# Performance work log

Hardware: AMD Instinct MI355X
Metric: run time of the kernel (lower is better)

## Reference

```python
import jax, jax.numpy as jnp
import numpy as np

B, T, H, W, C = 2, 8, 64, 64, 192
WIN = (4, 8, 8)
SHIFT = (2, 4, 4)
HEADS = 6
HID = 4 * C
N = WIN[0] * WIN[1] * WIN[2]  # 256 tokens per window
CPB_HID = 512


def window_partition(x, win):
    b, t, h, w, c = x.shape
    x = x.reshape(b, t // win[0], win[0], h // win[1], win[1], w // win[2], win[2], c)
    x = x.transpose(0, 1, 3, 5, 2, 4, 6, 7)
    return x.reshape(-1, win[0] * win[1] * win[2], c)


def window_reverse(wins, win, b, t, h, w):
    x = wins.reshape(b, t // win[0], h // win[1], w // win[2], win[0], win[1], win[2], -1)
    x = x.transpose(0, 1, 4, 2, 5, 3, 6, 7)
    return x.reshape(b, t, h, w, -1)


def _rel_coords_table():
    axes = [np.arange(-(WIN[i] - 1), WIN[i], dtype=np.float32) for i in range(3)]
    tbl = np.stack(np.meshgrid(*axes, indexing='ij'), axis=-1)  # (2wt-1,2wh-1,2ww-1,3)
    for i in range(3):
        tbl[..., i] /= WIN[i] - 1
    tbl *= 8.0
    tbl = np.sign(tbl) * np.log2(np.abs(tbl) + 1.0) / np.log2(8.0)
    return tbl.reshape(-1, 3)


def _rel_pos_index():
    coords = np.stack(np.meshgrid(np.arange(WIN[0]), np.arange(WIN[1]), np.arange(WIN[2]), indexing='ij'))
    cf = coords.reshape(3, -1)
    rel = (cf[:, :, None] - cf[:, None, :]).transpose(1, 2, 0)
    rel[..., 0] += WIN[0] - 1
    rel[..., 1] += WIN[1] - 1
    rel[..., 2] += WIN[2] - 1
    rel[..., 0] *= (2 * WIN[1] - 1) * (2 * WIN[2] - 1)
    rel[..., 1] *= 2 * WIN[2] - 1
    return rel.sum(-1)  # (N, N) int


def _attn_mask():
    img = np.zeros((1, T, H, W, 1), dtype=np.float32)
    cnt = 0
    for d in (slice(-WIN[0]), slice(-WIN[0], -SHIFT[0]), slice(-SHIFT[0], None)):
        for h in (slice(-WIN[1]), slice(-WIN[1], -SHIFT[1]), slice(-SHIFT[1], None)):
            for w in (slice(-WIN[2]), slice(-WIN[2], -SHIFT[2]), slice(-SHIFT[2], None)):
                img[:, d, h, w, :] = cnt
                cnt += 1
    mw = window_partition(img, WIN).squeeze(-1)  # (nW, N)
    am = mw[:, None, :] - mw[:, :, None]
    return np.where(am != 0, -100.0, 0.0).astype(np.float32)


REL_TABLE = jnp.asarray(_rel_coords_table())      # (M, 3)
RPI = jnp.asarray(_rel_pos_index().reshape(-1))   # (N*N,)
MASK = jnp.asarray(_attn_mask())                  # (nW, N, N)


def _ln(x, g, b):
    m = x.mean(-1, keepdims=True)
    v = x.var(-1, keepdims=True)
    return (x - m) / jnp.sqrt(v + 1e-5) * g + b


def setup_inputs() -> dict:
    key = jax.random.key(0)
    ks = jax.random.split(key, 16)
    s = lambda fan: 1.0 / np.sqrt(fan)
    return {
        'x': jax.random.normal(ks[0], (B, T, H, W, C), jnp.float32),
        'qkv_w': jax.random.normal(ks[1], (3 * C, C), jnp.float32) * s(C),
        'qkv_b': jnp.zeros((3 * C,), jnp.float32),
        'proj_w': jax.random.normal(ks[2], (C, C), jnp.float32) * s(C),
        'proj_b': jnp.zeros((C,), jnp.float32),
        'cpb_w1': jax.random.normal(ks[3], (CPB_HID, 3), jnp.float32) * s(3),
        'cpb_b1': jnp.zeros((CPB_HID,), jnp.float32),
        'cpb_w2': jax.random.normal(ks[4], (HEADS, CPB_HID), jnp.float32) * s(CPB_HID),
        'logit_scale': jnp.log(10.0 * jnp.ones((HEADS, 1, 1), jnp.float32)),
        'norm1_g': jnp.ones((C,), jnp.float32),
        'norm1_b': jnp.zeros((C,), jnp.float32),
        'norm2_g': jnp.ones((C,), jnp.float32),
        'norm2_b': jnp.zeros((C,), jnp.float32),
        'fc1_w': jax.random.normal(ks[5], (HID, C), jnp.float32) * s(C),
        'fc1_b': jnp.zeros((HID,), jnp.float32),
        'fc2_w': jax.random.normal(ks[6], (C, HID), jnp.float32) * s(HID),
        'fc2_b': jnp.zeros((C,), jnp.float32),
    }


def reference(x, qkv_w, qkv_b, proj_w, proj_b, cpb_w1, cpb_b1, cpb_w2,
              logit_scale, norm1_g, norm1_b, norm2_g, norm2_b,
              fc1_w, fc1_b, fc2_w, fc2_b):
    shortcut = x
    # cyclic shift
    xs = jnp.roll(x, shift=(-SHIFT[0], -SHIFT[1], -SHIFT[2]), axis=(1, 2, 3))
    xw = window_partition(xs, WIN)  # (B*nW, N, C)
    B_ = xw.shape[0]
    d = C // HEADS
    qkv = (xw @ qkv_w.T + qkv_b).reshape(B_, N, 3, HEADS, d).transpose(2, 0, 3, 1, 4)
    q, k, v = qkv[0], qkv[1], qkv[2]  # (B_, h, N, d)
    # cosine attention (F.normalize eps=1e-12)
    qn = q / jnp.maximum(jnp.linalg.norm(q, axis=-1, keepdims=True), 1e-12)
    kn = k / jnp.maximum(jnp.linalg.norm(k, axis=-1, keepdims=True), 1e-12)
    attn = jnp.einsum('bhnd,bhmd->bhnm', qn, kn)
    scale = jnp.exp(jnp.minimum(logit_scale, jnp.log(100.0)))  # clamp at log(1/0.01)
    attn = attn * scale
    # continuous relative position bias
    tbl = jax.nn.relu(REL_TABLE @ cpb_w1.T + cpb_b1) @ cpb_w2.T  # (M, heads)
    bias = tbl[RPI].reshape(N, N, HEADS).transpose(2, 0, 1)      # (h, N, N)
    attn = attn + 16.0 * jax.nn.sigmoid(bias)[None]
    # shift mask
    nW = MASK.shape[0]
    attn = attn.reshape(B_ // nW, nW, HEADS, N, N) + MASK[None, :, None]
    attn = jax.nn.softmax(attn.reshape(B_, HEADS, N, N), axis=-1)
    out = jnp.einsum('bhnm,bhmd->bhnd', attn, v)
    out = out.transpose(0, 2, 1, 3).reshape(B_, N, C)
    out = out @ proj_w.T + proj_b
    xr = window_reverse(out, WIN, B, T, H, W)
    xr = jnp.roll(xr, shift=SHIFT, axis=(1, 2, 3))
    # SwinV2 res-post-norm residual
    x = shortcut + _ln(xr, norm1_g, norm1_b)
    h1 = jax.nn.gelu(x @ fc1_w.T + fc1_b, approximate=False)
    x = x + _ln(h1 @ fc2_w.T + fc2_b, norm2_g, norm2_b)
    return x
```

## Files before the change

### kernel.cpp

```cpp
#include <hip/hip_runtime.h>
#include <math.h>


typedef short short8 __attribute__((ext_vector_type(8)));
typedef short short4v __attribute__((ext_vector_type(4)));
typedef float f32x4 __attribute__((ext_vector_type(4)));

__device__ __forceinline__ short f2bf(float f) {
    union { float f; unsigned u; } v; v.f = f;
    unsigned r = v.u + 0x7FFF + ((v.u >> 16) & 1);
    return (short)(r >> 16);
}

__device__ __forceinline__ float gelu_fast(float x) {
    float s = x * x;
    float t = fmaf(0.044715f, s, 1.0f);
    float y = -1.5957691216057308f * x * t;
    return x / (1.0f + __expf(y));
}

__global__ __launch_bounds__(64) void pack_w_k(const float* __restrict__ w,
                                               short* __restrict__ dst, int K) {
    int lane = threadIdx.x;
    int ktn = K >> 5;
    int nt = blockIdx.x / ktn, kt = blockIdx.x % ktn;
    int r = lane & 15, q = lane >> 4;
    const float* src = w + (size_t)(nt * 16 + r) * K + kt * 32 + q * 8;
    short8 v;
#pragma unroll
    for (int j = 0; j < 8; j++) v[j] = f2bf(src[j]);
    ((short8*)dst)[(size_t)blockIdx.x * 64 + lane] = v;
}

__global__ __launch_bounds__(64) void cpb_table_k(const float* __restrict__ w1,
                                                  const float* __restrict__ b1,
                                                  const float* __restrict__ w2,
                                                  float* __restrict__ tbl6) {
    int m = blockIdx.x;
    int lane = threadIdx.x;
    int it = m / 225;
    int ih = (m / 15) % 15;
    int iw = m % 15;
    float r0 = (float)(it - 3) * (8.0f / 3.0f);
    float r1 = (float)(ih - 7) * (8.0f / 7.0f);
    float r2 = (float)(iw - 7) * (8.0f / 7.0f);
    float c0 = (r0 < 0.f ? -1.f : 1.f) * log2f(fabsf(r0) + 1.0f) * (1.0f / 3.0f);
    float c1 = (r1 < 0.f ? -1.f : 1.f) * log2f(fabsf(r1) + 1.0f) * (1.0f / 3.0f);
    float c2 = (r2 < 0.f ? -1.f : 1.f) * log2f(fabsf(r2) + 1.0f) * (1.0f / 3.0f);
    float hv[8];
#pragma unroll
    for (int j = 0; j < 8; j++) {
        int t = lane * 8 + j;
        hv[j] = fmaxf(0.0f, c0 * w1[3 * t] + c1 * w1[3 * t + 1] + c2 * w1[3 * t + 2] + b1[t]);
    }
#pragma unroll
    for (int head = 0; head < 6; head++) {
        float s = 0.f;
#pragma unroll
        for (int j = 0; j < 8; j++) s += hv[j] * w2[head * 512 + lane * 8 + j];
        s += __shfl_xor(s, 1);
        s += __shfl_xor(s, 2);
        s += __shfl_xor(s, 4);
        s += __shfl_xor(s, 8);
        s += __shfl_xor(s, 16);
        s += __shfl_xor(s, 32);
        if (lane == 0) tbl6[m * 6 + head] = s;
    }
}

__global__ __launch_bounds__(256) void bias_k(const float* __restrict__ tbl6,
                                              float* __restrict__ biasT) {
    int idx = blockIdx.x * 256 + threadIdx.x;
    int h = idx >> 16;
    int rem = idx & 65535;
    int jj = rem >> 8, ii = rem & 255;
    int dt = (ii >> 6) - (jj >> 6) + 3;
    int dh = ((ii >> 3) & 7) - ((jj >> 3) & 7) + 7;
    int dw = (ii & 7) - (jj & 7) + 7;
    int rel = dt * 225 + dh * 15 + dw;
    float v = tbl6[rel * 6 + h];
    biasT[idx] = 16.0f / (1.0f + expf(-v));
}

#define ZSTR 388
__global__ __launch_bounds__(256) void qkv_mfma_k(const float* __restrict__ x,
                                                  const short* __restrict__ wqp,
                                                  const float* __restrict__ qkv_b,
                                                  short* __restrict__ qbf,
                                                  short* __restrict__ kbf,
                                                  short* __restrict__ vtb) {
    __shared__ float Z[32 * ZSTR];
    int tid = threadIdx.x, lane = tid & 63, w = tid >> 6;
    int r = lane & 15, q = lane >> 4;
    int b_ = blockIdx.x >> 3, n0 = (blockIdx.x & 7) << 5;
    int b = b_ >> 7, win = b_ & 127;
    int wt = win >> 6, wh = (win >> 3) & 7, ww = win & 7;

    short8 af[2][6];
#pragma unroll
    for (int m = 0; m < 2; m++) {
        int n = n0 + m * 16 + r;
        int t0 = ((wt * 4 + (n >> 6)) + 2) & 7;
        int h0 = ((wh * 8 + ((n >> 3) & 7)) + 4) & 63;
        int w0 = ((ww * 8 + (n & 7)) + 4) & 63;
        const float* src = x + ((size_t)((b * 8 + t0) * 64 + h0) * 64 + w0) * 192 + q * 8;
#pragma unroll
        for (int kt = 0; kt < 6; kt++) {
            float4 x0 = *(const float4*)(src + kt * 32);
            float4 x1 = *(const float4*)(src + kt * 32 + 4);
            short8 v;
            v[0] = f2bf(x0.x); v[1] = f2bf(x0.y); v[2] = f2bf(x0.z); v[3] = f2bf(x0.w);
            v[4] = f2bf(x1.x); v[5] = f2bf(x1.y); v[6] = f2bf(x1.z); v[7] = f2bf(x1.w);
            af[m][kt] = v;
        }
    }

    for (int ntl = 0; ntl < 9; ntl++) {
        int nt = w * 9 + ntl;
        float bias = qkv_b[nt * 16 + r];
        short8 bfr[6];
#pragma unroll
        for (int kt = 0; kt < 6; kt++)
            bfr[kt] = ((const short8*)wqp)[(size_t)(nt * 6 + kt) * 64 + lane];
        f32x4 a0 = {bias, bias, bias, bias};
        f32x4 a1 = {bias, bias, bias, bias};
#pragma unroll
        for (int kt = 0; kt < 6; kt++) {
            a0 = __builtin_amdgcn_mfma_f32_16x16x32_bf16(af[0][kt], bfr[kt], a0, 0, 0, 0);
            a1 = __builtin_amdgcn_mfma_f32_16x16x32_bf16(af[1][kt], bfr[kt], a1, 0, 0, 0);
        }
        int col = nt * 16 + r;
        if (nt < 24) {
#pragma unroll
            for (int reg = 0; reg < 4; reg++) {
                Z[(q * 4 + reg) * ZSTR + col] = a0[reg];
                Z[(16 + q * 4 + reg) * ZSTR + col] = a1[reg];
            }
        } else {
            int ch = col - 384;
            int hh = ch >> 5, dd = ch & 31;
            short* vb = vtb + ((size_t)(b_ * 6 + hh) * 32 + dd) * 256 + n0;
            short4v p0, p1;
#pragma unroll
            for (int reg = 0; reg < 4; reg++) { p0[reg] = f2bf(a0[reg]); p1[reg] = f2bf(a1[reg]); }
            *(short4v*)(vb + q * 4) = p0;
            *(short4v*)(vb + 16 + q * 4) = p1;
        }
    }
    __syncthreads();
    for (int rw = tid; rw < 384; rw += 256) {
        int token = rw / 12, rr = rw - token * 12;
        int isq = rr < 6 ? 1 : 0;
        int h = isq ? rr : rr - 6;
        const float* rp = &Z[token * ZSTR + rr * 32];
        float ss = 0.f;
#pragma unroll
        for (int d = 0; d < 32; d++) ss += rp[d] * rp[d];
        float inv = 1.0f / fmaxf(sqrtf(ss), 1e-12f);
        short* dst = (isq ? qbf : kbf) + ((size_t)(b_ * 6 + h) * 256 + n0 + token) * 32;
#pragma unroll
        for (int d8 = 0; d8 < 4; d8++) {
            short8 v;
#pragma unroll
            for (int j = 0; j < 8; j++) v[j] = f2bf(rp[d8 * 8 + j] * inv);
            *(short8*)(dst + d8 * 8) = v;
        }
    }
}

#define KSTR 40
#define VSTR 264
#define PSTR 40
__global__ __launch_bounds__(256) void attn_mfma_k(const short* __restrict__ qbf,
                                                   const short* __restrict__ kbf,
                                                   const short* __restrict__ vtb,
                                                   const float* __restrict__ biasT,
                                                   const float* __restrict__ logit_scale,
                                                   float* __restrict__ att) {
    __shared__ short Ks[256 * KSTR];
    __shared__ short Vs[32 * VSTR];
    __shared__ short Ps[4][16 * PSTR];
    int tid = threadIdx.x, lane = tid & 63, w = tid >> 6;
    int r = lane & 15, q = lane >> 4;
    int b_ = blockIdx.x / 6, h = blockIdx.x % 6;
    size_t base = (size_t)(b_ * 6 + h) * 8192;

    const short8* kg = (const short8*)(kbf + base);
    const short8* vg = (const short8*)(vtb + base);
    for (int i = tid; i < 1024; i += 256) {
        short8 kv = kg[i];
        *(short8*)&Ks[(i >> 2) * KSTR + (i & 3) * 8] = kv;
        short8 vv = vg[i];
        *(short8*)&Vs[(i >> 5) * VSTR + (i & 31) * 8] = vv;
    }

    short8 qf[4];
#pragma unroll
    for (int mt = 0; mt < 4; mt++)
        qf[mt] = *(const short8*)(qbf + base + (size_t)(w * 64 + mt * 16 + r) * 32 + q * 8);

    float scale = __expf(fminf(logit_scale[h], 4.6051702f));
    float M = scale + 16.0f;
    int win = b_ & 127;
    int wt4 = (win >> 6) * 4, wh8 = ((win >> 3) & 7) * 8, ww8 = (win & 7) * 8;
    auto region = [&](int n) {
        int ts = wt4 + (n >> 6), hs = wh8 + ((n >> 3) & 7), wsv = ww8 + (n & 7);
        int rt = ts < 4 ? 0 : (ts < 6 ? 1 : 2);
        int rh = hs < 56 ? 0 : (hs < 60 ? 1 : 2);
        int rw = wsv < 56 ? 0 : (wsv < 60 ? 1 : 2);
        return rt * 9 + rh * 3 + rw;
    };
    int rowreg[4][4];
#pragma unroll
    for (int mt = 0; mt < 4; mt++)
#pragma unroll
        for (int reg = 0; reg < 4; reg++)
            rowreg[mt][reg] = region(w * 64 + mt * 16 + q * 4 + reg);

    f32x4 O[4][2];
    float lp[4][4];
#pragma unroll
    for (int mt = 0; mt < 4; mt++) {
        O[mt][0] = (f32x4){0.f, 0.f, 0.f, 0.f};
        O[mt][1] = (f32x4){0.f, 0.f, 0.f, 0.f};
#pragma unroll
        for (int reg = 0; reg < 4; reg++) lp[mt][reg] = 0.f;
    }
    __syncthreads();

    const float* bh = biasT + ((size_t)h << 16);
    for (int s = 0; s < 8; s++) {
        short8 kf0 = *(const short8*)&Ks[(s * 32 + r) * KSTR + q * 8];
        short8 kf1 = *(const short8*)&Ks[(s * 32 + 16 + r) * KSTR + q * 8];
        short8 vf0 = *(const short8*)&Vs[r * VSTR + s * 32 + q * 8];
        short8 vf1 = *(const short8*)&Vs[(16 + r) * VSTR + s * 32 + q * 8];
        int cr0 = region(s * 32 + r);
        int cr1 = region(s * 32 + 16 + r);
#pragma unroll
        for (int mt = 0; mt < 4; mt++) {
            f32x4 s0 = {0.f, 0.f, 0.f, 0.f};
            f32x4 s1 = {0.f, 0.f, 0.f, 0.f};
            s0 = __builtin_amdgcn_mfma_f32_16x16x32_bf16(qf[mt], kf0, s0, 0, 0, 0);
            s1 = __builtin_amdgcn_mfma_f32_16x16x32_bf16(qf[mt], kf1, s1, 0, 0, 0);
            int qcol = w * 64 + mt * 16 + q * 4;
            float4 b0 = *(const float4*)(bh + (size_t)(s * 32 + r) * 256 + qcol);
            float4 b1 = *(const float4*)(bh + (size_t)(s * 32 + 16 + r) * 256 + qcol);
#pragma unroll
            for (int reg = 0; reg < 4; reg++) {
                float bb0 = (reg == 0 ? b0.x : reg == 1 ? b0.y : reg == 2 ? b0.z : b0.w);
                float bb1 = (reg == 0 ? b1.x : reg == 1 ? b1.y : reg == 2 ? b1.z : b1.w);
                float v0 = s0[reg] * scale + bb0 + (cr0 == rowreg[mt][reg] ? 0.f : -100.f) - M;
                float v1 = s1[reg] * scale + bb1 + (cr1 == rowreg[mt][reg] ? 0.f : -100.f) - M;
                float p0 = __expf(v0);
                float p1 = __expf(v1);
                lp[mt][reg] += p0 + p1;
                Ps[w][(q * 4 + reg) * PSTR + r] = f2bf(p0);
                Ps[w][(q * 4 + reg) * PSTR + 16 + r] = f2bf(p1);
            }
            short8 pa = *(const short8*)&Ps[w][r * PSTR + q * 8];
            O[mt][0] = __builtin_amdgcn_mfma_f32_16x16x32_bf16(pa, vf0, O[mt][0], 0, 0, 0);
            O[mt][1] = __builtin_amdgcn_mfma_f32_16x16x32_bf16(pa, vf1, O[mt][1], 0, 0, 0);
        }
    }

#pragma unroll
    for (int mt = 0; mt < 4; mt++)
#pragma unroll
        for (int reg = 0; reg < 4; reg++) {
            float v = lp[mt][reg];
            v += __shfl_xor(v, 1);
            v += __shfl_xor(v, 2);
            v += __shfl_xor(v, 4);
            v += __shfl_xor(v, 8);
            lp[mt][reg] = 1.0f / v;
        }
#pragma unroll
    for (int mt = 0; mt < 4; mt++)
#pragma unroll
        for (int nt = 0; nt < 2; nt++)
#pragma unroll
            for (int reg = 0; reg < 4; reg++) {
                int query = w * 64 + mt * 16 + q * 4 + reg;
                att[((size_t)b_ * 256 + query) * 192 + h * 32 + nt * 16 + r] =
                    O[mt][nt][reg] * lp[mt][reg];
            }
}

__global__ __launch_bounds__(256) void proj_mfma_k(const float* __restrict__ att,
                                                   const short* __restrict__ wpp,
                                                   const float* __restrict__ proj_b,
                                                   const float* __restrict__ x,
                                                   const float* __restrict__ g1,
                                                   const float* __restrict__ b1n,
                                                   float* __restrict__ out) {
    __shared__ float Z[32 * 196];
    __shared__ float ps[32][8];
    __shared__ float pss[32][8];
    __shared__ float mean_s[32], inv_s[32];
    int tid = threadIdx.x, lane = tid & 63, w = tid >> 6;
    int r = lane & 15, q = lane >> 4;
    int b_ = blockIdx.x >> 3, n0 = (blockIdx.x & 7) << 5;

    short8 af[2][6];
#pragma unroll
    for (int m = 0; m < 2; m++) {
        const float* src = att + ((size_t)b_ * 256 + n0 + m * 16 + r) * 192 + q * 8;
#pragma unroll
        for (int kt = 0; kt < 6; kt++) {
            float4 x0 = *(const float4*)(src + kt * 32);
            float4 x1 = *(const float4*)(src + kt * 32 + 4);
            short8 v;
            v[0] = f2bf(x0.x); v[1] = f2bf(x0.y); v[2] = f2bf(x0.z); v[3] = f2bf(x0.w);
            v[4] = f2bf(x1.x); v[5] = f2bf(x1.y); v[6] = f2bf(x1.z); v[7] = f2bf(x1.w);
            af[m][kt] = v;
        }
    }
    for (int ntl = 0; ntl < 3; ntl++) {
        int nt = w * 3 + ntl;
        float bias = proj_b[nt * 16 + r];
        short8 bfr[6];
#pragma unroll
        for (int kt = 0; kt < 6; kt++)
            bfr[kt] = ((const short8*)wpp)[(size_t)(nt * 6 + kt) * 64 + lane];
        f32x4 a0 = {bias, bias, bias, bias};
        f32x4 a1 = {bias, bias, bias, bias};
#pragma unroll
        for (int kt = 0; kt < 6; kt++) {
            a0 = __builtin_amdgcn_mfma_f32_16x16x32_bf16(af[0][kt], bfr[kt], a0, 0, 0, 0);
            a1 = __builtin_amdgcn_mfma_f32_16x16x32_bf16(af[1][kt], bfr[kt], a1, 0, 0, 0);
        }
        int col = nt * 16 + r;
#pragma unroll
        for (int reg = 0; reg < 4; reg++) {
            Z[(q * 4 + reg) * 196 + col] = a0[reg];
            Z[(16 + q * 4 + reg) * 196 + col] = a1[reg];
        }
    }
    __syncthreads();
    {
        int token = tid >> 3, part = tid & 7;
        float s = 0.f, ss = 0.f;
        const float* zr = &Z[token * 196 + part * 24];
#pragma unroll
        for (int c = 0; c < 24; c++) { float v = zr[c]; s += v; ss += v * v; }
        ps[token][part] = s; pss[token][part] = ss;
    }
    __syncthreads();
    if (tid < 32) {
        float s = 0.f, ss = 0.f;
#pragma unroll
        for (int p = 0; p < 8; p++) { s += ps[tid][p]; ss += pss[tid][p]; }
        float mean = s * (1.0f / 192.0f);
        float var = ss * (1.0f / 192.0f) - mean * mean;
        mean_s[tid] = mean;
        inv_s[tid] = 1.0f / sqrtf(var + 1e-5f);
    }
    __syncthreads();
    int b = b_ >> 7, win = b_ & 127;
    int wt = win >> 6, wh = (win >> 3) & 7, ww = win & 7;
    for (int idx = tid; idx < 6144; idx += 256) {
        int token = idx / 192;
        int ch = idx - token * 192;
        int n = n0 + token;
        int t0 = ((wt * 4 + (n >> 6)) + 2) & 7;
        int h0 = ((wh * 8 + ((n >> 3) & 7)) + 4) & 63;
        int w0 = ((ww * 8 + (n & 7)) + 4) & 63;
        size_t gb = ((size_t)((b * 8 + t0) * 64 + h0) * 64 + w0) * 192;
        float v = (Z[token * 196 + ch] - mean_s[token]) * inv_s[token] * g1[ch] + b1n[ch];
        out[gb + ch] = x[gb + ch] + v;
    }
}

#define HSTR 776
__global__ __launch_bounds__(512) void mlp_mfma_k(const short* __restrict__ w1p,
                                                  const short* __restrict__ w2p,
                                                  const float* __restrict__ fc1_b,
                                                  const float* __restrict__ fc2_b,
                                                  const float* __restrict__ g2,
                                                  const float* __restrict__ b2,
                                                  float* __restrict__ out) {
    __shared__ short Hs[32 * HSTR];
    __shared__ float ps[32][16];
    __shared__ float pss[32][16];
    __shared__ float mean_s[32], inv_s[32];
    int tid = threadIdx.x;
    int lane = tid & 63, w = tid >> 6;
    int r = lane & 15, q = lane >> 4;
    size_t tok0 = (size_t)blockIdx.x * 32;

    short8 af[2][6];
#pragma unroll
    for (int m = 0; m < 2; m++)
#pragma unroll
        for (int kt = 0; kt < 6; kt++) {
            const float* src = out + (tok0 + m * 16 + r) * 192 + kt * 32 + q * 8;
            float4 x0 = *(const float4*)src;
            float4 x1 = *(const float4*)(src + 4);
            short8 v;
            v[0] = f2bf(x0.x); v[1] = f2bf(x0.y); v[2] = f2bf(x0.z); v[3] = f2bf(x0.w);
            v[4] = f2bf(x1.x); v[5] = f2bf(x1.y); v[6] = f2bf(x1.z); v[7] = f2bf(x1.w);
            af[m][kt] = v;
        }

    for (int ntl = 0; ntl < 6; ntl++) {
        int nt = w * 6 + ntl;
        float bias = fc1_b[nt * 16 + r];
        short8 bfr[6];
#pragma unroll
        for (int kt = 0; kt < 6; kt++)
            bfr[kt] = ((const short8*)w1p)[(size_t)(nt * 6 + kt) * 64 + lane];
        f32x4 acc0 = {bias, bias, bias, bias};
        f32x4 acc1 = {bias, bias, bias, bias};
#pragma unroll
        for (int kt = 0; kt < 6; kt++) {
            acc0 = __builtin_amdgcn_mfma_f32_16x16x32_bf16(af[0][kt], bfr[kt], acc0, 0, 0, 0);
            acc1 = __builtin_amdgcn_mfma_f32_16x16x32_bf16(af[1][kt], bfr[kt], acc1, 0, 0, 0);
        }
        int col = nt * 16 + r;
#pragma unroll
        for (int reg = 0; reg < 4; reg++) {
            Hs[(q * 4 + reg) * HSTR + col] = f2bf(gelu_fast(acc0[reg]));
            Hs[(16 + q * 4 + reg) * HSTR + col] = f2bf(gelu_fast(acc1[reg]));
        }
    }
    __syncthreads();

    int odd = w & 1;
    int ntA = (3 * w) >> 1, ntB = ntA + 1;
    f32x4 acc2[3];
#pragma unroll
    for (int i = 0; i < 3; i++) acc2[i] = (f32x4){0.f, 0.f, 0.f, 0.f};
    for (int kk = 0; kk < 24; kk++) {
        short8 a0 = *(const short8*)&Hs[r * HSTR + kk * 32 + q * 8];
        short8 a1 = *(const short8*)&Hs[(16 + r) * HSTR + kk * 32 + q * 8];
        short8 bA = ((const short8*)w2p)[(size_t)(ntA * 24 + kk) * 64 + lane];
        short8 bB = ((const short8*)w2p)[(size_t)(ntB * 24 + kk) * 64 + lane];
        if (!odd) {
            acc2[0] = __builtin_amdgcn_mfma_f32_16x16x32_bf16(a0, bA, acc2[0], 0, 0, 0);
            acc2[1] = __builtin_amdgcn_mfma_f32_16x16x32_bf16(a1, bA, acc2[1], 0, 0, 0);
            acc2[2] = __builtin_amdgcn_mfma_f32_16x16x32_bf16(a0, bB, acc2[2], 0, 0, 0);
        } else {
            acc2[0] = __builtin_amdgcn_mfma_f32_16x16x32_bf16(a1, bA, acc2[0], 0, 0, 0);
            acc2[1] = __builtin_amdgcn_mfma_f32_16x16x32_bf16(a0, bB, acc2[1], 0, 0, 0);
            acc2[2] = __builtin_amdgcn_mfma_f32_16x16x32_bf16(a1, bB, acc2[2], 0, 0, 0);
        }
    }
    __syncthreads();
    float* Z = (float*)Hs;
    {
        int tnts[3], tms[3];
        tnts[0] = ntA; tms[0] = odd;
        tnts[1] = odd ? ntB : ntA; tms[1] = odd ? 0 : 1;
        tnts[2] = ntB; tms[2] = odd;
#pragma unroll
        for (int i = 0; i < 3; i++) {
            int col = tnts[i] * 16 + r;
            float bias2 = fc2_b[col];
#pragma unroll
            for (int reg = 0; reg < 4; reg++)
                Z[(tms[i] * 16 + q * 4 + reg) * 193 + col] = acc2[i][reg] + bias2;
        }
    }
    __syncthreads();

    {
        int token = tid >> 4, part = tid & 15;
        float s = 0.f, ss = 0.f;
        const float* zr = &Z[token * 193 + part * 12];
#pragma unroll
        for (int c = 0; c < 12; c++) { float v = zr[c]; s += v; ss += v * v; }
        ps[token][part] = s; pss[token][part] = ss;
    }
    __syncthreads();
    if (tid < 32) {
        float s = 0.f, ss = 0.f;
#pragma unroll
        for (int p = 0; p < 16; p++) { s += ps[tid][p]; ss += pss[tid][p]; }
        float mean = s * (1.0f / 192.0f);
        float var = ss * (1.0f / 192.0f) - mean * mean;
        mean_s[tid] = mean;
        inv_s[tid] = 1.0f / sqrtf(var + 1e-5f);
    }
    __syncthreads();
    for (int rep = 0; rep < 12; rep++) {
        int idx = rep * 512 + tid;
        int token = idx / 192;
        int ch = idx - token * 192;
        float v = (Z[token * 193 + ch] - mean_s[token]) * inv_s[token] * g2[ch] + b2[ch];
        size_t gi = (tok0 + token) * 192 + ch;
        out[gi] = out[gi] + v;
    }
}

extern "C" void kernel_launch(void* const* d_in, const int* in_sizes, int n_in,
                              void* d_out, int out_size, void* d_ws, size_t ws_size,
                              hipStream_t stream) {
    const float* x           = (const float*)d_in[0];
    const float* qkv_w       = (const float*)d_in[1];
    const float* qkv_b       = (const float*)d_in[2];
    const float* proj_w      = (const float*)d_in[3];
    const float* proj_b      = (const float*)d_in[4];
    const float* cpb_w1      = (const float*)d_in[5];
    const float* cpb_b1      = (const float*)d_in[6];
    const float* cpb_w2      = (const float*)d_in[7];
    const float* logit_scale = (const float*)d_in[8];
    const float* norm1_g     = (const float*)d_in[9];
    const float* norm1_b     = (const float*)d_in[10];
    const float* norm2_g     = (const float*)d_in[11];
    const float* norm2_b     = (const float*)d_in[12];
    const float* fc1_w       = (const float*)d_in[13];
    const float* fc1_b       = (const float*)d_in[14];
    const float* fc2_w       = (const float*)d_in[15];
    const float* fc2_b       = (const float*)d_in[16];
    float* out = (float*)d_out;

    float* ws = (float*)d_ws;
    const size_t QKVE = (size_t)256 * 6 * 256 * 32;
    float* att    = ws;
    float* biasT  = att + QKVE;
    float* tbl6   = biasT + (size_t)6 * 256 * 256;
    short* w1pack = (short*)(tbl6 + 9472);
    short* w2pack = w1pack + (size_t)768 * 192;
    short* wqpack = w2pack + (size_t)192 * 768;
    short* wppack = wqpack + (size_t)576 * 192;
    short* qbf    = wppack + (size_t)192 * 192;
    short* kbf    = qbf + QKVE;
    short* vtb    = kbf + QKVE;

    hipLaunchKernelGGL(pack_w_k, dim3(288), dim3(64), 0, stream, fc1_w, w1pack, 192);
    hipLaunchKernelGGL(pack_w_k, dim3(288), dim3(64), 0, stream, fc2_w, w2pack, 768);
    hipLaunchKernelGGL(pack_w_k, dim3(216), dim3(64), 0, stream, qkv_w, wqpack, 192);
    hipLaunchKernelGGL(pack_w_k, dim3(72), dim3(64), 0, stream, proj_w, wppack, 192);
    hipLaunchKernelGGL(cpb_table_k, dim3(1575), dim3(64), 0, stream, cpb_w1, cpb_b1, cpb_w2, tbl6);
    hipLaunchKernelGGL(bias_k, dim3(1536), dim3(256), 0, stream, tbl6, biasT);
    hipLaunchKernelGGL(qkv_mfma_k, dim3(2048), dim3(256), 0, stream, x, wqpack, qkv_b, qbf, kbf, vtb);
    hipLaunchKernelGGL(attn_mfma_k, dim3(1536), dim3(256), 0, stream, qbf, kbf, vtb, biasT, logit_scale, att);
    hipLaunchKernelGGL(proj_mfma_k, dim3(2048), dim3(256), 0, stream, att, wppack, proj_b, x, norm1_g, norm1_b, out);
    hipLaunchKernelGGL(mlp_mfma_k, dim3(2048), dim3(512), 0, stream, w1pack, w2pack,
                       fc1_b, fc2_b, norm2_g, norm2_b, out);
}
```

Measured before the change: 430.9 us.

## Emit bf16 copy of residual in proj, prefetch weights and vectorize MLP stores

The proj kernel now also writes a bf16 copy of the post-attention residual, so the MLP kernel loads bf16 activations directly instead of reading fp32 and converting. MFMA operands are swapped so each lane holds four consecutive columns, which allows vectorized f32x4 and short4 stores to LDS and vector bias loads. Weight fragments for fc1 and fc2 are double-buffered so the next tile is prefetched during the current MFMAs, and launch bounds request four blocks per CU. The extra bf16 buffer adds a global write in proj, and the prefetch registers may raise register pressure.

```diff
diff --git a/kernel.cpp b/kernel.cpp
--- a/kernel.cpp
+++ b/kernel.cpp
@@ -292,7 +292,8 @@
                                                    const float* __restrict__ x,
                                                    const float* __restrict__ g1,
                                                    const float* __restrict__ b1n,
-                                                   float* __restrict__ out) {
+                                                   float* __restrict__ out,
+                                                   short* __restrict__ xmb) {
     __shared__ float Z[32 * 196];
     __shared__ float ps[32][8];
     __shared__ float pss[32][8];
@@ -317,24 +318,19 @@
     }
     for (int ntl = 0; ntl < 3; ntl++) {
         int nt = w * 3 + ntl;
-        float bias = proj_b[nt * 16 + r];
+        f32x4 binit = *(const f32x4*)(proj_b + nt * 16 + q * 4);
         short8 bfr[6];
 #pragma unroll
         for (int kt = 0; kt < 6; kt++)
             bfr[kt] = ((const short8*)wpp)[(size_t)(nt * 6 + kt) * 64 + lane];
-        f32x4 a0 = {bias, bias, bias, bias};
-        f32x4 a1 = {bias, bias, bias, bias};
+        f32x4 a0 = binit, a1 = binit;
 #pragma unroll
         for (int kt = 0; kt < 6; kt++) {
-            a0 = __builtin_amdgcn_mfma_f32_16x16x32_bf16(af[0][kt], bfr[kt], a0, 0, 0, 0);
-            a1 = __builtin_amdgcn_mfma_f32_16x16x32_bf16(af[1][kt], bfr[kt], a1, 0, 0, 0);
-        }
-        int col = nt * 16 + r;
-#pragma unroll
-        for (int reg = 0; reg < 4; reg++) {
-            Z[(q * 4 + reg) * 196 + col] = a0[reg];
-            Z[(16 + q * 4 + reg) * 196 + col] = a1[reg];
-        }
+            a0 = __builtin_amdgcn_mfma_f32_16x16x32_bf16(bfr[kt], af[0][kt], a0, 0, 0, 0);
+            a1 = __builtin_amdgcn_mfma_f32_16x16x32_bf16(bfr[kt], af[1][kt], a1, 0, 0, 0);
+        }
+        *(f32x4*)&Z[(r) * 196 + nt * 16 + q * 4] = a0;
+        *(f32x4*)&Z[(16 + r) * 196 + nt * 16 + q * 4] = a1;
     }
     __syncthreads();
     {
@@ -367,18 +363,21 @@
         int w0 = ((ww * 8 + (n & 7)) + 4) & 63;
         size_t gb = ((size_t)((b * 8 + t0) * 64 + h0) * 64 + w0) * 192;
         float v = (Z[token * 196 + ch] - mean_s[token]) * inv_s[token] * g1[ch] + b1n[ch];
-        out[gb + ch] = x[gb + ch] + v;
+        float o = x[gb + ch] + v;
+        out[gb + ch] = o;
+        xmb[gb + ch] = f2bf(o);
     }
 }
 
 #define HSTR 776
-__global__ __launch_bounds__(512) void mlp_mfma_k(const short* __restrict__ w1p,
-                                                  const short* __restrict__ w2p,
-                                                  const float* __restrict__ fc1_b,
-                                                  const float* __restrict__ fc2_b,
-                                                  const float* __restrict__ g2,
-                                                  const float* __restrict__ b2,
-                                                  float* __restrict__ out) {
+__global__ __launch_bounds__(512, 4) void mlp_mfma_k(const short* __restrict__ xmb,
+                                                     const short* __restrict__ w1p,
+                                                     const short* __restrict__ w2p,
+                                                     const float* __restrict__ fc1_b,
+                                                     const float* __restrict__ fc2_b,
+                                                     const float* __restrict__ g2,
+                                                     const float* __restrict__ b2,
+                                                     float* __restrict__ out) {
     __shared__ short Hs[32 * HSTR];
     __shared__ float ps[32][16];
     __shared__ float pss[32][16];
@@ -392,35 +391,37 @@
 #pragma unroll
     for (int m = 0; m < 2; m++)
 #pragma unroll
-        for (int kt = 0; kt < 6; kt++) {
-            const float* src = out + (tok0 + m * 16 + r) * 192 + kt * 32 + q * 8;
-            float4 x0 = *(const float4*)src;
-            float4 x1 = *(const float4*)(src + 4);
-            short8 v;
-            v[0] = f2bf(x0.x); v[1] = f2bf(x0.y); v[2] = f2bf(x0.z); v[3] = f2bf(x0.w);
-            v[4] = f2bf(x1.x); v[5] = f2bf(x1.y); v[6] = f2bf(x1.z); v[7] = f2bf(x1.w);
-            af[m][kt] = v;
-        }
-
-    for (int ntl = 0; ntl < 6; ntl++) {
-        int nt = w * 6 + ntl;
-        float bias = fc1_b[nt * 16 + r];
-        short8 bfr[6];
-#pragma unroll
         for (int kt = 0; kt < 6; kt++)
-            bfr[kt] = ((const short8*)w1p)[(size_t)(nt * 6 + kt) * 64 + lane];
-        f32x4 acc0 = {bias, bias, bias, bias};
-        f32x4 acc1 = {bias, bias, bias, bias};
-#pragma unroll
-        for (int kt = 0; kt < 6; kt++) {
-            acc0 = __builtin_amdgcn_mfma_f32_16x16x32_bf16(af[0][kt], bfr[kt], acc0, 0, 0, 0);
-            acc1 = __builtin_amdgcn_mfma_f32_16x16x32_bf16(af[1][kt], bfr[kt], acc1, 0, 0, 0);
-        }
-        int col = nt * 16 + r;
-#pragma unroll
-        for (int reg = 0; reg < 4; reg++) {
-            Hs[(q * 4 + reg) * HSTR + col] = f2bf(gelu_fast(acc0[reg]));
-            Hs[(16 + q * 4 + reg) * HSTR + col] = f2bf(gelu_fast(acc1[reg]));
+            af[m][kt] = *(const short8*)(xmb + (tok0 + m * 16 + r) * 192 + kt * 32 + q * 8);
+
+    {
+        short8 bw[2][6];
+        int nt0 = w * 6;
+#pragma unroll
+        for (int kt = 0; kt < 6; kt++)
+            bw[0][kt] = ((const short8*)w1p)[(size_t)(nt0 * 6 + kt) * 64 + lane];
+        for (int ntl = 0; ntl < 6; ntl++) {
+            int nt = nt0 + ntl;
+            int cur = ntl & 1, nxt = cur ^ 1;
+            int ntn = (ntl < 5) ? nt + 1 : nt;
+#pragma unroll
+            for (int kt = 0; kt < 6; kt++)
+                bw[nxt][kt] = ((const short8*)w1p)[(size_t)(ntn * 6 + kt) * 64 + lane];
+            f32x4 binit = *(const f32x4*)(fc1_b + nt * 16 + q * 4);
+            f32x4 acc0 = binit, acc1 = binit;
+#pragma unroll
+            for (int kt = 0; kt < 6; kt++) {
+                acc0 = __builtin_amdgcn_mfma_f32_16x16x32_bf16(bw[cur][kt], af[0][kt], acc0, 0, 0, 0);
+                acc1 = __builtin_amdgcn_mfma_f32_16x16x32_bf16(bw[cur][kt], af[1][kt], acc1, 0, 0, 0);
+            }
+            short4v p0, p1;
+#pragma unroll
+            for (int reg = 0; reg < 4; reg++) {
+                p0[reg] = f2bf(gelu_fast(acc0[reg]));
+                p1[reg] = f2bf(gelu_fast(acc1[reg]));
+            }
+            *(short4v*)&Hs[(r) * HSTR + nt * 16 + q * 4] = p0;
+            *(short4v*)&Hs[(16 + r) * HSTR + nt * 16 + q * 4] = p1;
         }
     }
     __syncthreads();
@@ -430,19 +431,25 @@
     f32x4 acc2[3];
 #pragma unroll
     for (int i = 0; i < 3; i++) acc2[i] = (f32x4){0.f, 0.f, 0.f, 0.f};
-    for (int kk = 0; kk < 24; kk++) {
-        short8 a0 = *(const short8*)&Hs[r * HSTR + kk * 32 + q * 8];
-        short8 a1 = *(const short8*)&Hs[(16 + r) * HSTR + kk * 32 + q * 8];
-        short8 bA = ((const short8*)w2p)[(size_t)(ntA * 24 + kk) * 64 + lane];
-        short8 bB = ((const short8*)w2p)[(size_t)(ntB * 24 + kk) * 64 + lane];
-        if (!odd) {
-            acc2[0] = __builtin_amdgcn_mfma_f32_16x16x32_bf16(a0, bA, acc2[0], 0, 0, 0);
-            acc2[1] = __builtin_amdgcn_mfma_f32_16x16x32_bf16(a1, bA, acc2[1], 0, 0, 0);
-            acc2[2] = __builtin_amdgcn_mfma_f32_16x16x32_bf16(a0, bB, acc2[2], 0, 0, 0);
-        } else {
-            acc2[0] = __builtin_amdgcn_mfma_f32_16x16x32_bf16(a1, bA, acc2[0], 0, 0, 0);
-            acc2[1] = __builtin_amdgcn_mfma_f32_16x16x32_bf16(a0, bB, acc2[1], 0, 0, 0);
-            acc2[2] = __builtin_amdgcn_mfma_f32_16x16x32_bf16(a1, bB, acc2[2], 0, 0, 0);
+    {
+        short8 bA = ((const short8*)w2p)[(size_t)(ntA * 24 + 0) * 64 + lane];
+        short8 bB = ((const short8*)w2p)[(size_t)(ntB * 24 + 0) * 64 + lane];
+        for (int kk = 0; kk < 24; kk++) {
+            int kn = (kk < 23) ? kk + 1 : kk;
+            short8 bAn = ((const short8*)w2p)[(size_t)(ntA * 24 + kn) * 64 + lane];
+            short8 bBn = ((const short8*)w2p)[(size_t)(ntB * 24 + kn) * 64 + lane];
+            short8 a0 = *(const short8*)&Hs[r * HSTR + kk * 32 + q * 8];
+            short8 a1 = *(const short8*)&Hs[(16 + r) * HSTR + kk * 32 + q * 8];
+            if (!odd) {
+                acc2[0] = __builtin_amdgcn_mfma_f32_16x16x32_bf16(bA, a0, acc2[0], 0, 0, 0);
+                acc2[1] = __builtin_amdgcn_mfma_f32_16x16x32_bf16(bA, a1, acc2[1], 0, 0, 0);
+                acc2[2] = __builtin_amdgcn_mfma_f32_16x16x32_bf16(bB, a0, acc2[2], 0, 0, 0);
+            } else {
+                acc2[0] = __builtin_amdgcn_mfma_f32_16x16x32_bf16(bA, a1, acc2[0], 0, 0, 0);
+                acc2[1] = __builtin_amdgcn_mfma_f32_16x16x32_bf16(bB, a0, acc2[1], 0, 0, 0);
+                acc2[2] = __builtin_amdgcn_mfma_f32_16x16x32_bf16(bB, a1, acc2[2], 0, 0, 0);
+            }
+            bA = bAn; bB = bBn;
         }
     }
     __syncthreads();
@@ -454,11 +461,9 @@
         tnts[2] = ntB; tms[2] = odd;
 #pragma unroll
         for (int i = 0; i < 3; i++) {
-            int col = tnts[i] * 16 + r;
-            float bias2 = fc2_b[col];
-#pragma unroll
-            for (int reg = 0; reg < 4; reg++)
-                Z[(tms[i] * 16 + q * 4 + reg) * 193 + col] = acc2[i][reg] + bias2;
+            f32x4 b4 = *(const f32x4*)(fc2_b + tnts[i] * 16 + q * 4);
+            f32x4 zv = acc2[i] + b4;
+            *(f32x4*)&Z[(tms[i] * 16 + r) * 196 + tnts[i] * 16 + q * 4] = zv;
         }
     }
     __syncthreads();
@@ -466,7 +471,7 @@
     {
         int token = tid >> 4, part = tid & 15;
         float s = 0.f, ss = 0.f;
-        const float* zr = &Z[token * 193 + part * 12];
+        const float* zr = &Z[token * 196 + part * 12];
 #pragma unroll
         for (int c = 0; c < 12; c++) { float v = zr[c]; s += v; ss += v * v; }
         ps[token][part] = s; pss[token][part] = ss;
@@ -486,7 +491,7 @@
         int idx = rep * 512 + tid;
         int token = idx / 192;
         int ch = idx - token * 192;
-        float v = (Z[token * 193 + ch] - mean_s[token]) * inv_s[token] * g2[ch] + b2[ch];
+        float v = (Z[token * 196 + ch] - mean_s[token]) * inv_s[token] * g2[ch] + b2[ch];
         size_t gi = (tok0 + token) * 192 + ch;
         out[gi] = out[gi] + v;
     }
@@ -526,6 +531,7 @@
     short* qbf    = wppack + (size_t)192 * 192;
     short* kbf    = qbf + QKVE;
     short* vtb    = kbf + QKVE;
+    short* xmb    = vtb + QKVE;
 
     hipLaunchKernelGGL(pack_w_k, dim3(288), dim3(64), 0, stream, fc1_w, w1pack, 192);
     hipLaunchKernelGGL(pack_w_k, dim3(288), dim3(64), 0, stream, fc2_w, w2pack, 768);
@@ -535,7 +541,7 @@
     hipLaunchKernelGGL(bias_k, dim3(1536), dim3(256), 0, stream, tbl6, biasT);
     hipLaunchKernelGGL(qkv_mfma_k, dim3(2048), dim3(256), 0, stream, x, wqpack, qkv_b, qbf, kbf, vtb);
     hipLaunchKernelGGL(attn_mfma_k, dim3(1536), dim3(256), 0, stream, qbf, kbf, vtb, biasT, logit_scale, att);
-    hipLaunchKernelGGL(proj_mfma_k, dim3(2048), dim3(256), 0, stream, att, wppack, proj_b, x, norm1_g, norm1_b, out);
-    hipLaunchKernelGGL(mlp_mfma_k, dim3(2048), dim3(512), 0, stream, w1pack, w2pack,
+    hipLaunchKernelGGL(proj_mfma_k, dim3(2048), dim3(256), 0, stream, att, wppack, proj_b, x, norm1_g, norm1_b, out, xmb);
+    hipLaunchKernelGGL(mlp_mfma_k, dim3(2048), dim3(512), 0, stream, xmb, w1pack, w2pack,
                        fc1_b, fc2_b, norm2_g, norm2_b, out);
 }
```

New measurement: 422.8 us. Within noise of the previous version (-1.9%).
